# Kernel optimization log

Measured on AMD Instinct MI355X. Metric: run time of the kernel, lower is better.

## Reference

```python
import jax, jax.numpy as jnp
import numpy as np

B, T, QD, AD = 64, 4096, 1024, 256
SCORE_MASK_VALUE = -1e30


def setup_inputs() -> dict:
    key = jax.random.key(0)
    k1, k2, k3, k4, k5 = jax.random.split(key, 5)
    query = jax.random.normal(k1, (B, QD), dtype=jnp.float32)
    processed_memory = jax.random.normal(k2, (B, T, AD), dtype=jnp.float32)
    mask = jax.random.randint(k3, (B, T), 0, 2).astype(bool)
    Wq = jax.random.normal(k4, (AD, QD), dtype=jnp.float32) * (1.0 / np.sqrt(QD))
    v = jax.random.normal(k5, (AD,), dtype=jnp.float32) * (1.0 / np.sqrt(AD))
    return {"query": query, "processed_memory": processed_memory, "mask": mask, "Wq": Wq, "v": v}


def reference(query, processed_memory, mask, Wq, v):
    # processed_query: (B, AD) -> broadcast over time
    processed_query = query @ Wq.T                      # (B, AD)
    hidden = jnp.tanh(processed_query[:, None, :] + processed_memory)  # (B, T, AD)
    energies = jnp.einsum('btd,d->bt', hidden, v)       # (B, T)
    energies = jnp.where(mask, SCORE_MASK_VALUE, energies)
    alignment = jax.nn.softmax(energies, axis=1)        # (B, T)
    return alignment
```

## Files before the change

kernel.cpp:

```cpp
#include <hip/hip_runtime.h>
#include <math.h>

#define B_  64
#define T_  4096
#define QD_ 1024
#define AD_ 256
#define MASKVAL (-1e30f)
#define LOG2E 1.44269504f

__device__ __forceinline__ float tanh_fast(float x) {
    float xc = fminf(fmaxf(x, -9.0f), 9.0f);
    float e  = __builtin_amdgcn_exp2f(xc * (2.0f * LOG2E));
    return (e - 1.0f) * __builtin_amdgcn_rcpf(e + 1.0f);
}

__global__ __launch_bounds__(256) void pq_kernel(const float* __restrict__ query,
                                                 const float* __restrict__ Wq,
                                                 float* __restrict__ pq) {
    const int wave = threadIdx.x >> 6;
    const int lane = threadIdx.x & 63;
    const int w = blockIdx.x * 4 + wave;
    const int b = w >> 8;
    const int d = w & 255;

    const float4* q4 = (const float4*)(query + (size_t)b * QD_);
    const float4* w4 = (const float4*)(Wq + (size_t)d * QD_);
    float sum = 0.f;
#pragma unroll
    for (int j = 0; j < QD_ / 4 / 64; ++j) {
        const float4 a = q4[j * 64 + lane];
        const float4 c = w4[j * 64 + lane];
        sum += a.x * c.x + a.y * c.y + a.z * c.z + a.w * c.w;
    }
#pragma unroll
    for (int off = 32; off > 0; off >>= 1)
        sum += __shfl_xor(sum, off, 64);
    if (lane == 0) pq[w] = sum;
}

__global__ __launch_bounds__(256) void energy_kernel(const float* __restrict__ pm,
                                                     const int*   __restrict__ mask,
                                                     const float* __restrict__ pq,
                                                     const float* __restrict__ v,
                                                     float* __restrict__ energies) {
    const int wave = threadIdx.x >> 6;
    const int lane = threadIdx.x & 63;
    const size_t grp = (size_t)blockIdx.x * 4 + wave;
    const size_t t0  = grp * 4;
    const int b = (int)(t0 >> 12);

    const int4 mk = ((const int4*)mask)[grp];
    const int msk0 = __builtin_amdgcn_readfirstlane(mk.x);
    const int msk1 = __builtin_amdgcn_readfirstlane(mk.y);
    const int msk2 = __builtin_amdgcn_readfirstlane(mk.z);
    const int msk3 = __builtin_amdgcn_readfirstlane(mk.w);
    const int msk[4] = {msk0, msk1, msk2, msk3};

    const float4 q  = ((const float4*)(pq + (size_t)b * AD_))[lane];
    const float4 vv = ((const float4*)v)[lane];

    const float4* pm4 = (const float4*)pm;
    float4 m[4];
#pragma unroll
    for (int i = 0; i < 4; ++i)
        if (!msk[i]) m[i] = pm4[(t0 + i) * (AD_ / 4) + lane];

    float res[4];
#pragma unroll
    for (int i = 0; i < 4; ++i) {
        if (msk[i]) { res[i] = MASKVAL; continue; }
        float e = tanh_fast(q.x + m[i].x) * vv.x
                + tanh_fast(q.y + m[i].y) * vv.y
                + tanh_fast(q.z + m[i].z) * vv.z
                + tanh_fast(q.w + m[i].w) * vv.w;
#pragma unroll
        for (int off = 32; off > 0; off >>= 1)
            e += __shfl_xor(e, off, 64);
        res[i] = e;
    }
    if (lane == 0)
        ((float4*)energies)[grp] = make_float4(res[0], res[1], res[2], res[3]);
}

__global__ __launch_bounds__(512) void softmax_kernel(const float* __restrict__ energies,
                                                      float* __restrict__ out) {
    const int b    = blockIdx.x;
    const int tid  = threadIdx.x;
    const int wave = tid >> 6;
    const int lane = tid & 63;
    __shared__ float redmax[8];
    __shared__ float redsum[8];

    const float4* e4 = (const float4*)(energies + (size_t)b * T_);
    float4 v0 = e4[tid];
    float4 v1 = e4[tid + 512];

    float mx = fmaxf(fmaxf(fmaxf(v0.x, v0.y), fmaxf(v0.z, v0.w)),
                     fmaxf(fmaxf(v1.x, v1.y), fmaxf(v1.z, v1.w)));
#pragma unroll
    for (int off = 32; off > 0; off >>= 1)
        mx = fmaxf(mx, __shfl_xor(mx, off, 64));
    if (lane == 0) redmax[wave] = mx;
    __syncthreads();
#pragma unroll
    for (int i = 0; i < 8; ++i) mx = fmaxf(mx, redmax[i]);

    v0.x = __builtin_amdgcn_exp2f((v0.x - mx) * LOG2E);
    v0.y = __builtin_amdgcn_exp2f((v0.y - mx) * LOG2E);
    v0.z = __builtin_amdgcn_exp2f((v0.z - mx) * LOG2E);
    v0.w = __builtin_amdgcn_exp2f((v0.w - mx) * LOG2E);
    v1.x = __builtin_amdgcn_exp2f((v1.x - mx) * LOG2E);
    v1.y = __builtin_amdgcn_exp2f((v1.y - mx) * LOG2E);
    v1.z = __builtin_amdgcn_exp2f((v1.z - mx) * LOG2E);
    v1.w = __builtin_amdgcn_exp2f((v1.w - mx) * LOG2E);
    float s = v0.x + v0.y + v0.z + v0.w + v1.x + v1.y + v1.z + v1.w;
#pragma unroll
    for (int off = 32; off > 0; off >>= 1)
        s += __shfl_xor(s, off, 64);
    if (lane == 0) redsum[wave] = s;
    __syncthreads();
    s = 0.f;
#pragma unroll
    for (int i = 0; i < 8; ++i) s += redsum[i];

    const float inv = 1.f / s;
    float4* o4 = (float4*)(out + (size_t)b * T_);
    v0.x *= inv; v0.y *= inv; v0.z *= inv; v0.w *= inv;
    v1.x *= inv; v1.y *= inv; v1.z *= inv; v1.w *= inv;
    o4[tid]       = v0;
    o4[tid + 512] = v1;
}

extern "C" void kernel_launch(void* const* d_in, const int* in_sizes, int n_in,
                              void* d_out, int out_size, void* d_ws, size_t ws_size,
                              hipStream_t stream) {
    const float* query = (const float*)d_in[0];
    const float* pm    = (const float*)d_in[1];
    const int*   mask  = (const int*)  d_in[2];
    const float* Wq    = (const float*)d_in[3];
    const float* v     = (const float*)d_in[4];
    float* out = (float*)d_out;

    float* pq       = (float*)d_ws;
    float* energies = pq + (size_t)B_ * AD_;

    pq_kernel<<<(B_ * AD_) / 4, 256, 0, stream>>>(query, Wq, pq);
    energy_kernel<<<(B_ * T_) / 16, 256, 0, stream>>>(pm, mask, pq, v, energies);
    softmax_kernel<<<B_, 512, 0, stream>>>(energies, out);
}
```

Before: 341.8 us.

## Fuse exp and row-sum into energy kernel, replace softmax with scale pass

The energy kernel now applies exp directly to each energy without subtracting a row max, writes the exponentials, and accumulates per-row sums through a block-level reduction plus one atomicAdd per block into padded row-sum slots. The two-pass softmax kernel becomes a simple elementwise scale by the inverse row sum across many blocks. This removes the max reduction and the 64-block softmax launch with its low parallelism, at the cost of a memset, atomic contention on 64 addresses, and overflow risk because the energies are not max-shifted (they stay bounded by the norm of v, which keeps it safe in practice).

```diff
diff --git a/kernel.cpp b/kernel.cpp
--- a/kernel.cpp
+++ b/kernel.cpp
@@ -7,6 +7,7 @@
 #define AD_ 256
 #define MASKVAL (-1e30f)
 #define LOG2E 1.44269504f
+#define RS_STRIDE 32
 
 __device__ __forceinline__ float tanh_fast(float x) {
     float xc = fminf(fmaxf(x, -9.0f), 9.0f);
@@ -42,12 +43,14 @@
                                                      const int*   __restrict__ mask,
                                                      const float* __restrict__ pq,
                                                      const float* __restrict__ v,
-                                                     float* __restrict__ energies) {
+                                                     float* __restrict__ expv,
+                                                     float* __restrict__ rowsum) {
     const int wave = threadIdx.x >> 6;
     const int lane = threadIdx.x & 63;
     const size_t grp = (size_t)blockIdx.x * 4 + wave;
     const size_t t0  = grp * 4;
     const int b = (int)(t0 >> 12);
+    __shared__ float wsum[4];
 
     const int4 mk = ((const int4*)mask)[grp];
     const int msk0 = __builtin_amdgcn_readfirstlane(mk.x);
@@ -68,7 +71,7 @@
     float res[4];
 #pragma unroll
     for (int i = 0; i < 4; ++i) {
-        if (msk[i]) { res[i] = MASKVAL; continue; }
+        if (msk[i]) { res[i] = 0.0f; continue; }
         float e = tanh_fast(q.x + m[i].x) * vv.x
                 + tanh_fast(q.y + m[i].y) * vv.y
                 + tanh_fast(q.z + m[i].z) * vv.z
@@ -76,59 +79,26 @@
 #pragma unroll
         for (int off = 32; off > 0; off >>= 1)
             e += __shfl_xor(e, off, 64);
-        res[i] = e;
+        res[i] = __builtin_amdgcn_exp2f(e * LOG2E);
     }
-    if (lane == 0)
-        ((float4*)energies)[grp] = make_float4(res[0], res[1], res[2], res[3]);
+    if (lane == 0) {
+        ((float4*)expv)[grp] = make_float4(res[0], res[1], res[2], res[3]);
+        wsum[wave] = res[0] + res[1] + res[2] + res[3];
+    }
+    __syncthreads();
+    if (threadIdx.x == 0)
+        atomicAdd(&rowsum[b * RS_STRIDE], wsum[0] + wsum[1] + wsum[2] + wsum[3]);
 }
 
-__global__ __launch_bounds__(512) void softmax_kernel(const float* __restrict__ energies,
-                                                      float* __restrict__ out) {
-    const int b    = blockIdx.x;
-    const int tid  = threadIdx.x;
-    const int wave = tid >> 6;
-    const int lane = tid & 63;
-    __shared__ float redmax[8];
-    __shared__ float redsum[8];
-
-    const float4* e4 = (const float4*)(energies + (size_t)b * T_);
-    float4 v0 = e4[tid];
-    float4 v1 = e4[tid + 512];
-
-    float mx = fmaxf(fmaxf(fmaxf(v0.x, v0.y), fmaxf(v0.z, v0.w)),
-                     fmaxf(fmaxf(v1.x, v1.y), fmaxf(v1.z, v1.w)));
-#pragma unroll
-    for (int off = 32; off > 0; off >>= 1)
-        mx = fmaxf(mx, __shfl_xor(mx, off, 64));
-    if (lane == 0) redmax[wave] = mx;
-    __syncthreads();
-#pragma unroll
-    for (int i = 0; i < 8; ++i) mx = fmaxf(mx, redmax[i]);
-
-    v0.x = __builtin_amdgcn_exp2f((v0.x - mx) * LOG2E);
-    v0.y = __builtin_amdgcn_exp2f((v0.y - mx) * LOG2E);
-    v0.z = __builtin_amdgcn_exp2f((v0.z - mx) * LOG2E);
-    v0.w = __builtin_amdgcn_exp2f((v0.w - mx) * LOG2E);
-    v1.x = __builtin_amdgcn_exp2f((v1.x - mx) * LOG2E);
-    v1.y = __builtin_amdgcn_exp2f((v1.y - mx) * LOG2E);
-    v1.z = __builtin_amdgcn_exp2f((v1.z - mx) * LOG2E);
-    v1.w = __builtin_amdgcn_exp2f((v1.w - mx) * LOG2E);
-    float s = v0.x + v0.y + v0.z + v0.w + v1.x + v1.y + v1.z + v1.w;
-#pragma unroll
-    for (int off = 32; off > 0; off >>= 1)
-        s += __shfl_xor(s, off, 64);
-    if (lane == 0) redsum[wave] = s;
-    __syncthreads();
-    s = 0.f;
-#pragma unroll
-    for (int i = 0; i < 8; ++i) s += redsum[i];
-
-    const float inv = 1.f / s;
-    float4* o4 = (float4*)(out + (size_t)b * T_);
-    v0.x *= inv; v0.y *= inv; v0.z *= inv; v0.w *= inv;
-    v1.x *= inv; v1.y *= inv; v1.z *= inv; v1.w *= inv;
-    o4[tid]       = v0;
-    o4[tid + 512] = v1;
+__global__ __launch_bounds__(256) void scale_kernel(const float* __restrict__ expv,
+                                                    const float* __restrict__ rowsum,
+                                                    float* __restrict__ out) {
+    const size_t i = (size_t)blockIdx.x * 256 + threadIdx.x;
+    const int b = (int)(i >> 10);
+    const float inv = 1.0f / rowsum[b * RS_STRIDE];
+    float4 e = ((const float4*)expv)[i];
+    e.x *= inv; e.y *= inv; e.z *= inv; e.w *= inv;
+    ((float4*)out)[i] = e;
 }
 
 extern "C" void kernel_launch(void* const* d_in, const int* in_sizes, int n_in,
@@ -141,10 +111,12 @@
     const float* v     = (const float*)d_in[4];
     float* out = (float*)d_out;
 
-    float* pq       = (float*)d_ws;
-    float* energies = pq + (size_t)B_ * AD_;
+    float* pq     = (float*)d_ws;
+    float* expv   = pq + (size_t)B_ * AD_;
+    float* rowsum = expv + (size_t)B_ * T_;
 
+    hipMemsetAsync(rowsum, 0, B_ * RS_STRIDE * sizeof(float), stream);
     pq_kernel<<<(B_ * AD_) / 4, 256, 0, stream>>>(query, Wq, pq);
-    energy_kernel<<<(B_ * T_) / 16, 256, 0, stream>>>(pm, mask, pq, v, energies);
-    softmax_kernel<<<B_, 512, 0, stream>>>(energies, out);
+    energy_kernel<<<(B_ * T_) / 16, 256, 0, stream>>>(pm, mask, pq, v, expv, rowsum);
+    scale_kernel<<<(B_ * T_) / 1024, 256, 0, stream>>>(expv, rowsum, out);
 }
```

New measurement: 343.9 us. Within noise of the previous version (+0.6%).
